# Optimization experiments

Measured on AMD Instinct MI355X. Metric: run time of the kernel, lower is better.

The kernel has to match this reference:

```python
import jax, jax.numpy as jnp
import numpy as np

NB_CLASSES = 1024
SZ_EMBED = 128
N_SAMPLES = 262144
MRG = 0.1
ALPHA = 32.0


def l2_norm(x):
    # matches torch l2_norm: divide by sqrt(sum(x^2, dim=1) + 1e-12)
    return x / jnp.sqrt(jnp.sum(x * x, axis=1, keepdims=True) + 1e-12)


def setup_inputs() -> dict:
    key = jax.random.key(0)
    k1, k2, k3 = jax.random.split(key, 3)
    X = jax.random.normal(k1, (N_SAMPLES, SZ_EMBED), dtype=jnp.float32)
    proxies = jax.random.normal(k2, (NB_CLASSES, SZ_EMBED), dtype=jnp.float32)
    T = jax.random.randint(k3, (N_SAMPLES,), 0, NB_CLASSES)
    return {"X": X, "proxies": proxies, "T": T}


def reference(X, proxies, T):
    # cosine similarities: [N, C]
    cos = l2_norm(X) @ l2_norm(proxies).T
    # on-device one-hot replaces the numpy binarize roundtrip
    P_one_hot = jax.nn.one_hot(T, NB_CLASSES, dtype=cos.dtype)  # [N, C]
    pos_exp_w = jnp.exp(-ALPHA * (cos - MRG)) * P_one_hot
    neg_exp_w = jnp.exp(ALPHA * (cos + MRG)) * (1.0 - P_one_hot)
    P_sim_sum = pos_exp_w.sum(axis=0)  # [C]
    N_sim_sum = neg_exp_w.sum(axis=0)  # [C]
    num_valid = (P_one_hot.sum(axis=0) != 0).sum().astype(cos.dtype)
    pos_term = jnp.where(
        num_valid > 0,
        jnp.log1p(P_sim_sum).sum() / jnp.maximum(num_valid, 1.0),
        jnp.zeros((), cos.dtype),
    )
    neg_term = jnp.log1p(N_sim_sum).sum() / NB_CLASSES
    loss = pos_term + neg_term
    return jnp.stack([loss, pos_term, neg_term])
```

## Files before the change

### kernel.cpp

```cpp
#include <hip/hip_runtime.h>
#include <math.h>

#define NB_CLASSES 1024
#define SZ_EMBED 128
#define N_SAMPLES 262144
#define MTILE 64
#define CTILE 64
#define NBLOCKS (N_SAMPLES / MTILE)
#define XSTRIDE 136

typedef __bf16 v8bf __attribute__((ext_vector_type(8)));
typedef float v4f __attribute__((ext_vector_type(4)));

#define EXP_A 46.16624130844683f
#define EXP_B 4.616624130844683f

#define SMEM_BYTES 19712

__device__ __forceinline__ unsigned short f2bf(float f) {
    union { float f; unsigned u; } v; v.f = f;
    unsigned u = v.u;
    unsigned rounding = 0x7FFFu + ((u >> 16) & 1u);
    return (unsigned short)((u + rounding) >> 16);
}
__device__ __forceinline__ float bfbits_lo(unsigned u) {
    union { unsigned u; float f; } v; v.u = u << 16; return v.f;
}
__device__ __forceinline__ float bfbits_hi(unsigned u) {
    union { unsigned u; float f; } v; v.u = u & 0xffff0000u; return v.f;
}

__global__ __launch_bounds__(256) void norm_proxies_kernel(
    const float* __restrict__ proxies, unsigned short* __restrict__ pn) {
    int wv = threadIdx.x >> 6;
    int lane = threadIdx.x & 63;
    int row = blockIdx.x * 4 + wv;
    const float* src = proxies + (size_t)row * SZ_EMBED + lane * 2;
    float2 x = *(const float2*)src;
    float ss = x.x * x.x + x.y * x.y;
    #pragma unroll
    for (int off = 32; off; off >>= 1) ss += __shfl_xor(ss, off);
    float inv = rsqrtf(ss + 1e-12f);
    unsigned pk = (unsigned)f2bf(x.x * inv) | ((unsigned)f2bf(x.y * inv) << 16);
    *(unsigned*)(pn + (size_t)row * SZ_EMBED + lane * 2) = pk;
}

__global__ __launch_bounds__(256, 4) void main_kernel(
    const float* __restrict__ X, const int* __restrict__ T,
    const unsigned short* __restrict__ Pn,
    float* __restrict__ partial_neg, float* __restrict__ pos_g,
    float* __restrict__ negd_g) {
    __shared__ __align__(16) char smem[SMEM_BYTES];
    unsigned short* xtile = (unsigned short*)smem;
    float (*psum)[4] = (float(*)[4])(smem + 17408);
    float (*dsum)[4] = (float(*)[4])(smem + 18432);
    int* tT = (int*)(smem + 19456);

    const int t = threadIdx.x;
    const int lane = t & 63;
    const int wv = t >> 6;
    const int quad = lane >> 4;
    const int l15 = lane & 15;
    const int sample_base = blockIdx.x * MTILE;
    const int row = t >> 2, part = t & 3;

    {
        const float4* src = (const float4*)(X + (size_t)(sample_base + row) * SZ_EMBED + part * 32);
        float4 r[8];
        float ss = 0.f;
        #pragma unroll
        for (int j = 0; j < 8; ++j) {
            r[j] = src[j];
            ss += r[j].x * r[j].x + r[j].y * r[j].y + r[j].z * r[j].z + r[j].w * r[j].w;
        }
        psum[row][part] = ss;
        if (t < MTILE) tT[t] = T[sample_base + t];
        __syncthreads();
        float inv = rsqrtf(psum[row][0] + psum[row][1] + psum[row][2] + psum[row][3] + 1e-12f);
        unsigned short* dst = xtile + row * XSTRIDE + part * 32;
        #pragma unroll
        for (int j = 0; j < 8; ++j) {
            uint2 pk;
            pk.x = (unsigned)f2bf(r[j].x * inv) | ((unsigned)f2bf(r[j].y * inv) << 16);
            pk.y = (unsigned)f2bf(r[j].z * inv) | ((unsigned)f2bf(r[j].w * inv) << 16);
            *(uint2*)(dst + j * 4) = pk;
        }
        int lbl = tT[row];
        const unsigned short* prow = Pn + (size_t)lbl * SZ_EMBED + part * 32;
        float d = 0.f;
        #pragma unroll
        for (int j = 0; j < 4; ++j) {
            uint4 pv = *(const uint4*)(prow + j * 8);
            float4 xa = r[2 * j], xb = r[2 * j + 1];
            d += bfbits_lo(pv.x) * xa.x + bfbits_hi(pv.x) * xa.y;
            d += bfbits_lo(pv.y) * xa.z + bfbits_hi(pv.y) * xa.w;
            d += bfbits_lo(pv.z) * xb.x + bfbits_hi(pv.z) * xb.y;
            d += bfbits_lo(pv.w) * xb.z + bfbits_hi(pv.w) * xb.w;
        }
        dsum[row][part] = d * inv;
        __syncthreads();
        if (part == 0) {
            int lbl2 = tT[row];
            float dd = dsum[row][0] + dsum[row][1] + dsum[row][2] + dsum[row][3];
            float dp = __builtin_amdgcn_exp2f(fmaf(dd, -EXP_A, EXP_B));
            float dn = __builtin_amdgcn_exp2f(fmaf(dd,  EXP_A, EXP_B));
            atomicAdd(&pos_g[lbl2], dp);
            atomicAdd(&negd_g[lbl2], dn);
        }
    }

    v8bf afrag[4][4];
    #pragma unroll
    for (int ri = 0; ri < 4; ++ri)
        #pragma unroll
        for (int kc = 0; kc < 4; ++kc)
            afrag[ri][kc] = *(const v8bf*)(xtile + (ri * 16 + l15) * XSTRIDE + kc * 32 + quad * 8);

    const unsigned short* bptr = Pn + (size_t)(wv * 16 + l15) * SZ_EMBED + quad * 8;
    v8bf bfrag[4];
    #pragma unroll
    for (int kc = 0; kc < 4; ++kc)
        bfrag[kc] = *(const v8bf*)(bptr + kc * 32);

    float* nrow = partial_neg + (size_t)blockIdx.x * NB_CLASSES + wv * 16 + l15;

    #pragma unroll
    for (int ct = 0; ct < NB_CLASSES / CTILE; ++ct) {
        v4f zero = {0.f, 0.f, 0.f, 0.f};
        v4f acc[4] = {zero, zero, zero, zero};
        #pragma unroll
        for (int kc = 0; kc < 4; ++kc)
            #pragma unroll
            for (int ri = 0; ri < 4; ++ri)
                acc[ri] = __builtin_amdgcn_mfma_f32_16x16x32_bf16(afrag[ri][kc], bfrag[kc], acc[ri], 0, 0, 0);

        if (ct < NB_CLASSES / CTILE - 1) {
            const unsigned short* nb = bptr + (size_t)(ct + 1) * CTILE * SZ_EMBED;
            #pragma unroll
            for (int kc = 0; kc < 4; ++kc)
                bfrag[kc] = *(const v8bf*)(nb + kc * 32);
        }

        float e[16];
        #pragma unroll
        for (int ri = 0; ri < 4; ++ri)
            #pragma unroll
            for (int r = 0; r < 4; ++r)
                e[ri * 4 + r] = __builtin_amdgcn_exp2f(fmaf(acc[ri][r], EXP_A, EXP_B));
        #pragma unroll
        for (int s = 8; s; s >>= 1)
            #pragma unroll
            for (int j = 0; j < s; ++j)
                e[j] += e[j + s];
        float v = e[0];
        v += __shfl_xor(v, 16);
        v += __shfl_xor(v, 32);
        if (quad == 0) nrow[ct * CTILE] = v;
    }
}

__global__ __launch_bounds__(256) void row_reduce_kernel(float* __restrict__ partial_neg) {
    const int t = threadIdx.x;
    const int g = blockIdx.x >> 2, q = blockIdx.x & 3;
    float* base = partial_neg + (size_t)g * 64 * NB_CLASSES + q * 256 + t;
    float s = 0.f;
    #pragma unroll 8
    for (int r = 0; r < 64; ++r) s += base[(size_t)r * NB_CLASSES];
    base[0] = s;
}

__global__ __launch_bounds__(256) void finalize_kernel(
    const float* __restrict__ partial_neg, const float* __restrict__ pos_g,
    const float* __restrict__ negd_g, float* __restrict__ out) {
    int t = threadIdx.x;
    float4 ns = {0.f, 0.f, 0.f, 0.f};
    #pragma unroll 8
    for (int r = 0; r < 64; ++r) {
        float4 vn = *(const float4*)(partial_neg + (size_t)r * 64 * NB_CLASSES + 4 * t);
        ns.x += vn.x; ns.y += vn.y; ns.z += vn.z; ns.w += vn.w;
    }
    float4 nd = *(const float4*)(negd_g + 4 * t);
    ns.x -= nd.x; ns.y -= nd.y; ns.z -= nd.z; ns.w -= nd.w;
    float4 ps = *(const float4*)(pos_g + 4 * t);
    float lp_pos = log1pf(ps.x) + log1pf(ps.y) + log1pf(ps.z) + log1pf(ps.w);
    float lp_neg = log1pf(ns.x) + log1pf(ns.y) + log1pf(ns.z) + log1pf(ns.w);
    float valid = (ps.x != 0.f) + (ps.y != 0.f) + (ps.z != 0.f) + (ps.w != 0.f);
    #pragma unroll
    for (int off = 32; off; off >>= 1) {
        lp_pos += __shfl_xor(lp_pos, off);
        lp_neg += __shfl_xor(lp_neg, off);
        valid  += __shfl_xor(valid, off);
    }
    __shared__ float s[3][4];
    int wv = t >> 6, lane = t & 63;
    if (lane == 0) { s[0][wv] = lp_pos; s[1][wv] = lp_neg; s[2][wv] = valid; }
    __syncthreads();
    if (t == 0) {
        float P = s[0][0] + s[0][1] + s[0][2] + s[0][3];
        float Ng = s[1][0] + s[1][1] + s[1][2] + s[1][3];
        float V = s[2][0] + s[2][1] + s[2][2] + s[2][3];
        float pos_term = (V > 0.f) ? (P / fmaxf(V, 1.f)) : 0.f;
        float neg_term = Ng / (float)NB_CLASSES;
        out[0] = pos_term + neg_term;
        out[1] = pos_term;
        out[2] = neg_term;
    }
}

extern "C" void kernel_launch(void* const* d_in, const int* in_sizes, int n_in,
                              void* d_out, int out_size, void* d_ws, size_t ws_size,
                              hipStream_t stream) {
    const float* X = (const float*)d_in[0];
    const float* proxies = (const float*)d_in[1];
    const int* T = (const int*)d_in[2];
    float* out = (float*)d_out;

    char* ws = (char*)d_ws;
    unsigned short* Pn = (unsigned short*)ws;
    float* pos_g = (float*)(ws + (size_t)NB_CLASSES * SZ_EMBED * sizeof(unsigned short));
    float* negd_g = pos_g + NB_CLASSES;
    float* partial_neg = negd_g + NB_CLASSES;

    hipMemsetAsync(pos_g, 0, 2 * NB_CLASSES * sizeof(float), stream);
    norm_proxies_kernel<<<NB_CLASSES / 4, 256, 0, stream>>>(proxies, Pn);
    main_kernel<<<NBLOCKS, 256, 0, stream>>>(X, T, Pn, partial_neg, pos_g, negd_g);
    row_reduce_kernel<<<256, 256, 0, stream>>>(partial_neg);
    finalize_kernel<<<1, 256, 0, stream>>>(partial_neg, pos_g, negd_g, out);
}
```

Baseline: 324.6 us.

## Stage proxy tiles into swizzled LDS with async double buffering

```diff
diff --git a/kernel.cpp b/kernel.cpp
--- a/kernel.cpp
+++ b/kernel.cpp
@@ -15,7 +15,7 @@
 #define EXP_A 46.16624130844683f
 #define EXP_B 4.616624130844683f
 
-#define SMEM_BYTES 19712
+#define SMEM_BYTES 52480
 
 __device__ __forceinline__ unsigned short f2bf(float f) {
     union { float f; unsigned u; } v; v.f = f;
@@ -45,7 +45,7 @@
     *(unsigned*)(pn + (size_t)row * SZ_EMBED + lane * 2) = pk;
 }
 
-__global__ __launch_bounds__(256, 4) void main_kernel(
+__global__ __launch_bounds__(256) void main_kernel(
     const float* __restrict__ X, const int* __restrict__ T,
     const unsigned short* __restrict__ Pn,
     float* __restrict__ partial_neg, float* __restrict__ pos_g,
@@ -55,6 +55,7 @@
     float (*psum)[4] = (float(*)[4])(smem + 17408);
     float (*dsum)[4] = (float(*)[4])(smem + 18432);
     int* tT = (int*)(smem + 19456);
+    char* btile = smem + 19712;
 
     const int t = threadIdx.x;
     const int lane = t & 63;
@@ -63,6 +64,23 @@
     const int l15 = lane & 15;
     const int sample_base = blockIdx.x * MTILE;
     const int row = t >> 2, part = t & 3;
+    const char* PnB = (const char*)Pn;
+
+#define STAGE(tc, b) do {                                                      \
+        char* lb_ = btile + (b) * 16384 + wv * 4096;                           \
+        _Pragma("unroll")                                                      \
+        for (int c_ = 0; c_ < 4; ++c_) {                                       \
+            int rw_ = c_ * 4 + (lane >> 4);                                    \
+            const char* g_ = PnB + ((size_t)((tc) * 64 + wv * 16 + rw_)) * 256 \
+                             + (((lane & 15) * 16) ^ ((rw_ & 7) << 4));        \
+            __builtin_amdgcn_global_load_lds(                                  \
+                (__attribute__((address_space(1))) const void*)g_,             \
+                (__attribute__((address_space(3))) void*)(lb_ + c_ * 1024),    \
+                16, 0, 0);                                                     \
+        }                                                                      \
+    } while (0)
+
+    STAGE(0, 0);
 
     {
         const float4* src = (const float4*)(X + (size_t)(sample_base + row) * SZ_EMBED + part * 32);
@@ -116,16 +134,20 @@
         for (int kc = 0; kc < 4; ++kc)
             afrag[ri][kc] = *(const v8bf*)(xtile + (ri * 16 + l15) * XSTRIDE + kc * 32 + quad * 8);
 
-    const unsigned short* bptr = Pn + (size_t)(wv * 16 + l15) * SZ_EMBED + quad * 8;
-    v8bf bfrag[4];
-    #pragma unroll
-    for (int kc = 0; kc < 4; ++kc)
-        bfrag[kc] = *(const v8bf*)(bptr + kc * 32);
-
     float* nrow = partial_neg + (size_t)blockIdx.x * NB_CLASSES + wv * 16 + l15;
+    const int bswz = ((l15 & 7) << 4);
+    const char* brow_base = btile + (wv * 16 + l15) * 256;
 
     #pragma unroll
     for (int ct = 0; ct < NB_CLASSES / CTILE; ++ct) {
+        const int cur = ct & 1;
+        if (ct < NB_CLASSES / CTILE - 1) STAGE(ct + 1, cur ^ 1);
+
+        v8bf bfrag[4];
+        #pragma unroll
+        for (int kc = 0; kc < 4; ++kc)
+            bfrag[kc] = *(const v8bf*)(brow_base + cur * 16384 + ((kc * 64 + quad * 16) ^ bswz));
+
         v4f zero = {0.f, 0.f, 0.f, 0.f};
         v4f acc[4] = {zero, zero, zero, zero};
         #pragma unroll
@@ -133,13 +155,6 @@
             #pragma unroll
             for (int ri = 0; ri < 4; ++ri)
                 acc[ri] = __builtin_amdgcn_mfma_f32_16x16x32_bf16(afrag[ri][kc], bfrag[kc], acc[ri], 0, 0, 0);
-
-        if (ct < NB_CLASSES / CTILE - 1) {
-            const unsigned short* nb = bptr + (size_t)(ct + 1) * CTILE * SZ_EMBED;
-            #pragma unroll
-            for (int kc = 0; kc < 4; ++kc)
-                bfrag[kc] = *(const v8bf*)(nb + kc * 32);
-        }
 
         float e[16];
         #pragma unroll
@@ -156,7 +171,10 @@
         v += __shfl_xor(v, 16);
         v += __shfl_xor(v, 32);
         if (quad == 0) nrow[ct * CTILE] = v;
-    }
+
+        __syncthreads();
+    }
+#undef STAGE
 }
 
 __global__ __launch_bounds__(256) void row_reduce_kernel(float* __restrict__ partial_neg) {
```

After: 296.1 us. 1.1x faster.
